# Kernel tuning notes

Measured on AMD Instinct MI355X. Metric: run time of the kernel, lower is better.

Reference implementation:

```python
import jax, jax.numpy as jnp
import numpy as np

N_NODES = 200000
N_EDGES = 400000
N_GRAPHS = 4096
H = 300
L = 5
BN_EPS = 1e-5


def setup_inputs() -> dict:
    key = jax.random.key(0)
    ks = jax.random.split(key, 12)
    s = 0.05  # weight scale for numerical stability across 5 layers
    return {
        'x': jax.random.randint(ks[0], (N_NODES, 9), 0, 120),
        'edge_index': jax.random.randint(ks[1], (2, N_EDGES), 0, N_NODES),
        'edge_attr': jax.random.randint(ks[2], (N_EDGES, 3), 0, 16),
        'batch': jnp.sort(jax.random.randint(ks[3], (N_NODES,), 0, N_GRAPHS)),
        'atom_emb': jax.random.normal(ks[4], (9, 120, H), jnp.float32) * s,
        'bond_emb': jax.random.normal(ks[5], (L, 3, 16, H), jnp.float32) * s,
        'eps': jnp.zeros((L,), jnp.float32),
        'W1': jax.random.normal(ks[6], (L, H, 2 * H), jnp.float32) * s,
        'b1': jnp.zeros((L, 2 * H), jnp.float32),
        'bn_gamma': jnp.ones((L, 2 * H), jnp.float32),
        'bn_beta': jnp.zeros((L, 2 * H), jnp.float32),
        'bn_mean': jnp.zeros((L, 2 * H), jnp.float32),
        'bn_var': jnp.ones((L, 2 * H), jnp.float32),
        'W2': jax.random.normal(ks[7], (L, 2 * H, H), jnp.float32) * s,
        'b2': jnp.zeros((L, H), jnp.float32),
        'cls_W': jax.random.normal(ks[8], (H, 2), jnp.float32) * s,
        'cls_b': jnp.zeros((2,), jnp.float32),
    }


def reference(x, edge_index, edge_attr, batch, atom_emb, bond_emb, eps,
              W1, b1, bn_gamma, bn_beta, bn_mean, bn_var, W2, b2, cls_W, cls_b):
    N = x.shape[0]
    # AtomEncoder: sum of 9 categorical embeddings -> [N, H]
    h = jnp.sum(atom_emb[jnp.arange(9)[None, :], x], axis=1)
    src, dst = edge_index[0], edge_index[1]
    feat_idx3 = jnp.arange(3)[None, :]
    for l in range(W1.shape[0]):
        # BondEncoder for this layer: sum of 3 categorical embeddings -> [E, H]
        e = jnp.sum(bond_emb[l][feat_idx3, edge_attr], axis=1)
        # message = relu(x_j + edge_emb), aggregated by scatter-add at dst
        m = jax.nn.relu(h[src] + e)
        agg = jax.ops.segment_sum(m, dst, num_segments=N)
        z = (1.0 + eps[l]) * h + agg
        # MLP: Linear(H,2H) -> BN(eval) -> ReLU -> Linear(2H,H)
        z = z @ W1[l] + b1[l]
        z = (z - bn_mean[l]) * (bn_gamma[l] * jax.lax.rsqrt(bn_var[l] + BN_EPS)) + bn_beta[l]
        z = jax.nn.relu(z)
        h = z @ W2[l] + b2[l]
    # global mean pool over graphs
    sums = jax.ops.segment_sum(h, batch, num_segments=N_GRAPHS)
    counts = jax.ops.segment_sum(jnp.ones((N, 1), h.dtype), batch, num_segments=N_GRAPHS)
    graph_feature = sums / jnp.maximum(counts, 1.0)
    logits = graph_feature @ cls_W + cls_b
    return logits, graph_feature
```

## Files before the change

### kernel.cpp

```cpp
#include <hip/hip_runtime.h>
#include <hip/hip_bf16.h>

#define N_NODES 200000
#define N_EDGES 400000
#define N_GRAPHS 4096
#define HDIM 300
#define H2DIM 600
#define NLAYERS 5

typedef __hip_bfloat16 bf16;
typedef __attribute__((ext_vector_type(4))) short s16x4;
typedef __attribute__((ext_vector_type(8))) short s16x8;
typedef __attribute__((ext_vector_type(4))) float f32x4v;

__device__ inline short f2bf(float f) {
    __hip_bfloat16 b = __float2bfloat16(f);
    return *(short*)&b;
}
__device__ inline float bf2f(short s) {
    __hip_bfloat16 b = *(__hip_bfloat16*)&s;
    return __bfloat162float(b);
}

__device__ inline void gload_lds16(const short* g, short* l) {
    __builtin_amdgcn_global_load_lds(
        (const __attribute__((address_space(1))) unsigned int*)g,
        (__attribute__((address_space(3))) unsigned int*)l,
        16, 0, 0);
}

__global__ void diag_kernel(float* __restrict__ out, int n, float val) {
    int i = blockIdx.x * blockDim.x + threadIdx.x;
    if (i < n) out[i] = val;
}

__global__ void hist_kernel(const int* __restrict__ edge_index, int* __restrict__ offs) {
    int e = blockIdx.x * blockDim.x + threadIdx.x;
    if (e >= N_EDGES) return;
    atomicAdd(&offs[edge_index[N_EDGES + e]], 1);
}

#define SCAN_N 200001
__global__ void scan1_kernel(int* __restrict__ offs, int* __restrict__ bsum) {
    __shared__ int ls[256];
    int tid = threadIdx.x;
    int base = blockIdx.x * 1024 + tid * 4;
    int v[4];
#pragma unroll
    for (int j = 0; j < 4; j++) v[j] = (base + j < SCAN_N) ? offs[base + j] : 0;
    int t = v[0] + v[1] + v[2] + v[3];
    ls[tid] = t;
    __syncthreads();
    for (int off = 1; off < 256; off <<= 1) {
        int y = (tid >= off) ? ls[tid - off] : 0;
        __syncthreads();
        ls[tid] += y;
        __syncthreads();
    }
    int ex = ls[tid] - t;
#pragma unroll
    for (int j = 0; j < 4; j++) {
        if (base + j < SCAN_N) offs[base + j] = ex;
        ex += v[j];
    }
    if (tid == 255) bsum[blockIdx.x] = ls[255];
}

__global__ void scan2_kernel(int* __restrict__ bsum, int nb) {
    __shared__ int ls[256];
    int tid = threadIdx.x;
    int v = (tid < nb) ? bsum[tid] : 0;
    ls[tid] = v;
    __syncthreads();
    for (int off = 1; off < 256; off <<= 1) {
        int y = (tid >= off) ? ls[tid - off] : 0;
        __syncthreads();
        ls[tid] += y;
        __syncthreads();
    }
    if (tid < nb) bsum[tid] = ls[tid] - v;
}

__global__ void scan3_kernel(int* __restrict__ offs, const int* __restrict__ bsum) {
    int i = blockIdx.x * blockDim.x + threadIdx.x;
    if (i >= SCAN_N) return;
    offs[i] += bsum[i >> 10];
}

__global__ void scatter_kernel(const int* __restrict__ edge_index,
                               const int* __restrict__ edge_attr,
                               int* __restrict__ offs,
                               int* __restrict__ sidx) {
    int e = blockIdx.x * blockDim.x + threadIdx.x;
    if (e >= N_EDGES) return;
    int src = edge_index[e];
    int dst = edge_index[N_EDGES + e];
    int combo = edge_attr[e * 3 + 0] | (edge_attr[e * 3 + 1] << 4) | (edge_attr[e * 3 + 2] << 8);
    int pos = atomicAdd(&offs[dst], 1);
    sidx[pos] = src | (combo << 18);
}

__global__ void etab_kernel(const float* __restrict__ bond_l, short* __restrict__ etab) {
    int idx = blockIdx.x * blockDim.x + threadIdx.x;
    if (idx >= 4096 * 304) return;
    int combo = idx / 304;
    int c = idx - combo * 304;
    if (c >= HDIM) { etab[idx] = 0; return; }
    int a0 = combo & 15, a1 = (combo >> 4) & 15, a2 = combo >> 8;
    float v = bond_l[a0 * HDIM + c] + bond_l[16 * HDIM + a1 * HDIM + c]
            + bond_l[32 * HDIM + a2 * HDIM + c];
    etab[idx] = f2bf(v);
}

__global__ void prep_w_swz(const float* __restrict__ W1, const float* __restrict__ W2,
                           short* __restrict__ Wt1s, short* __restrict__ Wt2s) {
    int idx = blockIdx.x * blockDim.x + threadIdx.x;
    const int G1 = NLAYERS * 40 * 10 * 64;
    const int G2 = NLAYERS * 20 * 20 * 64;
    if (idx < G1) {
        int l = idx / (40 * 10 * 64);
        int r = idx - l * (40 * 10 * 64);
        int nt = r / (10 * 64);
        int r2 = r - nt * (10 * 64);
        int kb = r2 >> 6;
        int lane = r2 & 63;
        int n = nt * 16 + (lane & 15);
        int k0 = kb * 32 + (lane >> 4) * 8;
        s16x8 o;
#pragma unroll
        for (int j = 0; j < 8; j++) {
            int k = k0 + j;
            float v = (n < H2DIM && k < HDIM) ? W1[((size_t)l * HDIM + k) * H2DIM + n] : 0.f;
            o[j] = f2bf(v);
        }
        *(s16x8*)&Wt1s[(size_t)idx * 8] = o;
    } else if (idx < G1 + G2) {
        int t = idx - G1;
        int l = t / (20 * 20 * 64);
        int r = t - l * (20 * 20 * 64);
        int nt = r / (20 * 64);
        int r2 = r - nt * (20 * 64);
        int kb = r2 >> 6;
        int lane = r2 & 63;
        int n = nt * 16 + (lane & 15);
        int k0 = kb * 32 + (lane >> 4) * 8;
        s16x8 o;
#pragma unroll
        for (int j = 0; j < 8; j++) {
            int k = k0 + j;
            float v = (n < HDIM && k < H2DIM) ? W2[((size_t)l * H2DIM + k) * HDIM + n] : 0.f;
            o[j] = f2bf(v);
        }
        *(s16x8*)&Wt2s[(size_t)t * 8] = o;
    }
}

__global__ void atom_kernel(const int* __restrict__ x,
                            const float* __restrict__ atom_emb,
                            short* __restrict__ h) {
    int i = blockIdx.x * blockDim.x + threadIdx.x;
    if (i >= N_NODES * 75) return;
    int n = i / 75;
    int c = (i - n * 75) * 4;
    const int* xr = x + n * 9;
    float4 s = {0.f, 0.f, 0.f, 0.f};
#pragma unroll
    for (int f = 0; f < 9; f++) {
        float4 v = *(const float4*)&atom_emb[(size_t)(f * 120 + xr[f]) * HDIM + c];
        s.x += v.x; s.y += v.y; s.z += v.z; s.w += v.w;
    }
    s16x4 o = {f2bf(s.x), f2bf(s.y), f2bf(s.z), f2bf(s.w)};
    *(s16x4*)&h[(size_t)n * HDIM + c] = o;
}

__launch_bounds__(256)
__global__ void agg_kernel(const short* __restrict__ h_in,
                           short* __restrict__ z,
                           const int* __restrict__ offs,
                           const int* __restrict__ sidx,
                           const short* __restrict__ etab,
                           const float* __restrict__ eps, int l) {
    int tid = threadIdx.x;
    int q = tid >> 4;
    int l16 = tid & 15;
    int n = blockIdx.x * 16 + q;
    float e1 = 1.f + eps[l];
    int beg = (n == 0) ? 0 : offs[n - 1];
    int end = offs[n];

    float4 acc[5];
#pragma unroll
    for (int j = 0; j < 5; j++) acc[j] = (float4){0.f, 0.f, 0.f, 0.f};
    bool tail = l16 < 11;
    int ctail = 256 + l16 * 4;

    int e = beg;
    for (; e + 2 <= end; e += 2) {
        int pk0 = sidx[e];
        int pk1 = sidx[e + 1];
        const short* hr0 = h_in + (size_t)(pk0 & 0x3FFFF) * HDIM;
        const short* er0 = etab + (((unsigned)pk0) >> 18) * 304;
        const short* hr1 = h_in + (size_t)(pk1 & 0x3FFFF) * HDIM;
        const short* er1 = etab + (((unsigned)pk1) >> 18) * 304;
        s16x4 hv0[5], ev0[5], hv1[5], ev1[5];
#pragma unroll
        for (int rep = 0; rep < 4; rep++) {
            int c = rep * 64 + l16 * 4;
            hv0[rep] = *(const s16x4*)(hr0 + c);
            ev0[rep] = *(const s16x4*)(er0 + c);
            hv1[rep] = *(const s16x4*)(hr1 + c);
            ev1[rep] = *(const s16x4*)(er1 + c);
        }
        if (tail) {
            hv0[4] = *(const s16x4*)(hr0 + ctail);
            ev0[4] = *(const s16x4*)(er0 + ctail);
            hv1[4] = *(const s16x4*)(hr1 + ctail);
            ev1[4] = *(const s16x4*)(er1 + ctail);
        }
#pragma unroll
        for (int rep = 0; rep < 5; rep++) {
            if (rep == 4 && !tail) continue;
            acc[rep].x += fmaxf(0.f, bf2f(hv0[rep].x) + bf2f(ev0[rep].x))
                        + fmaxf(0.f, bf2f(hv1[rep].x) + bf2f(ev1[rep].x));
            acc[rep].y += fmaxf(0.f, bf2f(hv0[rep].y) + bf2f(ev0[rep].y))
                        + fmaxf(0.f, bf2f(hv1[rep].y) + bf2f(ev1[rep].y));
            acc[rep].z += fmaxf(0.f, bf2f(hv0[rep].z) + bf2f(ev0[rep].z))
                        + fmaxf(0.f, bf2f(hv1[rep].z) + bf2f(ev1[rep].z));
            acc[rep].w += fmaxf(0.f, bf2f(hv0[rep].w) + bf2f(ev0[rep].w))
                        + fmaxf(0.f, bf2f(hv1[rep].w) + bf2f(ev1[rep].w));
        }
    }
    if (e < end) {
        int pk0 = sidx[e];
        const short* hr0 = h_in + (size_t)(pk0 & 0x3FFFF) * HDIM;
        const short* er0 = etab + (((unsigned)pk0) >> 18) * 304;
        s16x4 hv0[5], ev0[5];
#pragma unroll
        for (int rep = 0; rep < 4; rep++) {
            int c = rep * 64 + l16 * 4;
            hv0[rep] = *(const s16x4*)(hr0 + c);
            ev0[rep] = *(const s16x4*)(er0 + c);
        }
        if (tail) {
            hv0[4] = *(const s16x4*)(hr0 + ctail);
            ev0[4] = *(const s16x4*)(er0 + ctail);
        }
#pragma unroll
        for (int rep = 0; rep < 5; rep++) {
            if (rep == 4 && !tail) continue;
            acc[rep].x += fmaxf(0.f, bf2f(hv0[rep].x) + bf2f(ev0[rep].x));
            acc[rep].y += fmaxf(0.f, bf2f(hv0[rep].y) + bf2f(ev0[rep].y));
            acc[rep].z += fmaxf(0.f, bf2f(hv0[rep].z) + bf2f(ev0[rep].z));
            acc[rep].w += fmaxf(0.f, bf2f(hv0[rep].w) + bf2f(ev0[rep].w));
        }
    }

    const short* hn = h_in + (size_t)n * HDIM;
    short* zr = z + (size_t)n * HDIM;
#pragma unroll
    for (int rep = 0; rep < 5; rep++) {
        if (rep == 4 && !tail) continue;
        int c = rep < 4 ? rep * 64 + l16 * 4 : ctail;
        s16x4 hv = *(const s16x4*)(hn + c);
        s16x4 o;
        o.x = f2bf(fmaf(e1, bf2f(hv.x), acc[rep].x));
        o.y = f2bf(fmaf(e1, bf2f(hv.y), acc[rep].y));
        o.z = f2bf(fmaf(e1, bf2f(hv.z), acc[rep].z));
        o.w = f2bf(fmaf(e1, bf2f(hv.w), acc[rep].w));
        *(s16x4*)(zr + c) = o;
    }
}

#define ZST 328
#define WBUF_OFF (64 * ZST)
#define WBUF_SHORTS (20 * 64 * 8)
#define YS_OFF (WBUF_OFF + WBUF_SHORTS)
#define YST 136
#define LDS_SHORTS (YS_OFF + 64 * YST)

__launch_bounds__(256, 2)
__global__ void mlp_kernel(const short* __restrict__ zin,
                           short* __restrict__ hout,
                           const short* __restrict__ Wt1,
                           const short* __restrict__ Wt2,
                           const float* __restrict__ b1l,
                           const float* __restrict__ gammal,
                           const float* __restrict__ betal,
                           const float* __restrict__ meanl,
                           const float* __restrict__ varl,
                           const float* __restrict__ b2l) {
    __shared__ short lds[LDS_SHORTS];
    int tid = threadIdx.x;
    int wng = tid >> 6;
    int lane = tid & 63;
    int quad = lane >> 4;
    int l16 = lane & 15;
    int row0 = blockIdx.x * 64;

    for (int i = tid; i < 64 * 82; i += 256) {
        int r = i / 82;
        int p = (i - r * 82) * 4;
        s16x4 v = *(const s16x4*)&zin[(size_t)(row0 + r) * HDIM + p];
        *(s16x4*)&lds[r * ZST + p] = v;
    }

    f32x4v acc2[4][5];
#pragma unroll
    for (int rt = 0; rt < 4; rt++)
#pragma unroll
        for (int ct = 0; ct < 5; ct++) acc2[rt][ct] = (f32x4v){0.f, 0.f, 0.f, 0.f};

    for (int cc = 0; cc < 5; cc++) {
        f32x4v acc1[4][2];
#pragma unroll
        for (int rt = 0; rt < 4; rt++)
#pragma unroll
            for (int ct = 0; ct < 2; ct++) acc1[rt][ct] = (f32x4v){0.f, 0.f, 0.f, 0.f};

        for (int kbp = 0; kbp < 5; kbp++) {
            __syncthreads();
#pragma unroll
            for (int j = 0; j < 4; j++) {
                int c = j * 4 + wng;
                int nt_ = c >> 1, kb2 = c & 1;
                const short* src = Wt1 +
                    ((size_t)(((cc * 8 + nt_) * 10 + kbp * 2 + kb2) * 64) + lane) * 8;
                gload_lds16(src, &lds[WBUF_OFF + c * 512]);
            }
            __syncthreads();
#pragma unroll
            for (int kb2 = 0; kb2 < 2; kb2++) {
                int ks = (kbp * 2 + kb2) * 32 + quad * 8;
                s16x8 a[4];
#pragma unroll
                for (int rt = 0; rt < 4; rt++)
                    a[rt] = *(const s16x8*)&lds[(rt * 16 + l16) * ZST + ks];
#pragma unroll
                for (int ct = 0; ct < 2; ct++) {
                    int c = (wng * 2 + ct) * 2 + kb2;
                    s16x8 b = *(const s16x8*)&lds[WBUF_OFF + c * 512 + lane * 8];
#pragma unroll
                    for (int rt = 0; rt < 4; rt++)
                        acc1[rt][ct] = __builtin_amdgcn_mfma_f32_16x16x32_bf16(a[rt], b, acc1[rt][ct], 0, 0, 0);
                }
            }
        }
#pragma unroll
        for (int ct = 0; ct < 2; ct++) {
            int kc = wng * 32 + ct * 16 + l16;
            int col = cc * 128 + kc;
            bool valid = col < H2DIM;
            float s = 0.f, sh = 0.f;
            if (valid) {
                s = gammal[col] * rsqrtf(varl[col] + 1e-5f);
                sh = betal[col] + (b1l[col] - meanl[col]) * s;
            }
#pragma unroll
            for (int rt = 0; rt < 4; rt++)
#pragma unroll
                for (int rr = 0; rr < 4; rr++) {
                    float v = valid ? fmaxf(0.f, fmaf(acc1[rt][ct][rr], s, sh)) : 0.f;
                    lds[YS_OFF + (rt * 16 + quad * 4 + rr) * YST + kc] = f2bf(v);
                }
        }
#pragma unroll
        for (int kbl = 0; kbl < 4; kbl++) {
            __syncthreads();
#pragma unroll
            for (int j = 0; j < 5; j++) {
                int c = j * 4 + wng;
                const short* src = Wt2 +
                    ((size_t)((c * 20 + cc * 4 + kbl) * 64) + lane) * 8;
                gload_lds16(src, &lds[WBUF_OFF + c * 512]);
            }
            __syncthreads();
            int ks = kbl * 32 + quad * 8;
            s16x8 a[4];
#pragma unroll
            for (int rt = 0; rt < 4; rt++)
                a[rt] = *(const s16x8*)&lds[YS_OFF + (rt * 16 + l16) * YST + ks];
#pragma unroll
            for (int ct = 0; ct < 5; ct++) {
                int c = wng * 5 + ct;
                s16x8 b = *(const s16x8*)&lds[WBUF_OFF + c * 512 + lane * 8];
#pragma unroll
                for (int rt = 0; rt < 4; rt++)
                    acc2[rt][ct] = __builtin_amdgcn_mfma_f32_16x16x32_bf16(a[rt], b, acc2[rt][ct], 0, 0, 0);
            }
        }
    }
#pragma unroll
    for (int ct = 0; ct < 5; ct++) {
        int col = wng * 80 + ct * 16 + l16;
        if (col < HDIM) {
            float bb = b2l[col];
#pragma unroll
            for (int rt = 0; rt < 4; rt++)
#pragma unroll
                for (int rr = 0; rr < 4; rr++) {
                    int r = rt * 16 + quad * 4 + rr;
                    lds[r * HDIM + col] = f2bf(acc2[rt][ct][rr] + bb);
                }
        }
    }
    __syncthreads();
    for (int i = tid; i < 64 * 75; i += 256) {
        *(s16x4*)&hout[(size_t)row0 * HDIM + i * 4] = *(const s16x4*)&lds[i * 4];
    }
}

__device__ int lower_bound_dev(const int* a, int n, int v) {
    int lo = 0, hi = n;
    while (lo < hi) {
        int mid = (lo + hi) >> 1;
        if (a[mid] < v) lo = mid + 1; else hi = mid;
    }
    return lo;
}

__global__ void pool_kernel(const short* __restrict__ h,
                            const int* __restrict__ batch,
                            const float* __restrict__ cls_W,
                            const float* __restrict__ cls_b,
                            float* __restrict__ out) {
    __shared__ int seg[2];
    __shared__ float r0s[256], r1s[256];
    int g = blockIdx.x;
    int t = threadIdx.x;
    if (t == 0) {
        seg[0] = lower_bound_dev(batch, N_NODES, g);
        seg[1] = lower_bound_dev(batch, N_NODES, g + 1);
    }
    __syncthreads();
    int s = seg[0], e = seg[1];
    float inv = 1.f / fmaxf((float)(e - s), 1.f);
    float p0 = 0.f, p1 = 0.f;
    if (t < 75) {
        int c = t * 4;
        float4 sum = {0.f, 0.f, 0.f, 0.f};
        for (int n = s; n < e; n++) {
            s16x4 v = *(const s16x4*)&h[(size_t)n * HDIM + c];
            sum.x += bf2f(v.x);
            sum.y += bf2f(v.y);
            sum.z += bf2f(v.z);
            sum.w += bf2f(v.w);
        }
        float4 gf = {sum.x * inv, sum.y * inv, sum.z * inv, sum.w * inv};
        *(float4*)&out[2 * N_GRAPHS + (size_t)g * HDIM + c] = gf;
        p0 = gf.x * cls_W[c * 2] + gf.y * cls_W[(c + 1) * 2]
           + gf.z * cls_W[(c + 2) * 2] + gf.w * cls_W[(c + 3) * 2];
        p1 = gf.x * cls_W[c * 2 + 1] + gf.y * cls_W[(c + 1) * 2 + 1]
           + gf.z * cls_W[(c + 2) * 2 + 1] + gf.w * cls_W[(c + 3) * 2 + 1];
    }
    r0s[t] = p0;
    r1s[t] = p1;
    __syncthreads();
    for (int st = 128; st > 0; st >>= 1) {
        if (t < st) { r0s[t] += r0s[t + st]; r1s[t] += r1s[t + st]; }
        __syncthreads();
    }
    if (t == 0) {
        out[g * 2 + 0] = r0s[0] + cls_b[0];
        out[g * 2 + 1] = r1s[0] + cls_b[1];
    }
}

extern "C" void kernel_launch(void* const* d_in, const int* in_sizes, int n_in,
                              void* d_out, int out_size, void* d_ws, size_t ws_size,
                              hipStream_t stream) {
    const int* x          = (const int*)d_in[0];
    const int* edge_index = (const int*)d_in[1];
    const int* edge_attr  = (const int*)d_in[2];
    const int* batch      = (const int*)d_in[3];
    const float* atom_emb = (const float*)d_in[4];
    const float* bond_emb = (const float*)d_in[5];
    const float* eps      = (const float*)d_in[6];
    const float* W1       = (const float*)d_in[7];
    const float* b1       = (const float*)d_in[8];
    const float* bn_gamma = (const float*)d_in[9];
    const float* bn_beta  = (const float*)d_in[10];
    const float* bn_mean  = (const float*)d_in[11];
    const float* bn_var   = (const float*)d_in[12];
    const float* W2       = (const float*)d_in[13];
    const float* b2       = (const float*)d_in[14];
    const float* cls_W    = (const float*)d_in[15];
    const float* cls_b    = (const float*)d_in[16];
    float* out = (float*)d_out;

    char* base = (char*)d_ws;
    const size_t OFF_HA   = 0;
    const size_t OFF_HB   = 120000000;
    const size_t OFF_WT1  = 240000000;
    const size_t OFF_WT2  = 242048000;
    const size_t OFF_ETAB = 244096000;
    const size_t OFF_SIDX = 246586368;
    const size_t OFF_OFFS = 248186368;
    const size_t OFF_BSUM = 248986384;
    const size_t TOTAL    = 248987168;

    if (ws_size < TOTAL) {
        float mb = (float)(ws_size >> 20);
        diag_kernel<<<(out_size + 255) / 256, 256, 0, stream>>>(out, out_size, mb);
        return;
    }

    short* hA   = (short*)(base + OFF_HA);
    short* hB   = (short*)(base + OFF_HB);
    short* Wt1s = (short*)(base + OFF_WT1);
    short* Wt2s = (short*)(base + OFF_WT2);
    short* etab = (short*)(base + OFF_ETAB);
    int*   sidx = (int*)(base + OFF_SIDX);
    int*   offs = (int*)(base + OFF_OFFS);
    int*   bsum = (int*)(base + OFF_BSUM);

    hipMemsetAsync(offs, 0, SCAN_N * sizeof(int), stream);
    hist_kernel<<<(N_EDGES + 255) / 256, 256, 0, stream>>>(edge_index, offs);
    scan1_kernel<<<196, 256, 0, stream>>>(offs, bsum);
    scan2_kernel<<<1, 256, 0, stream>>>(bsum, 196);
    scan3_kernel<<<(SCAN_N + 255) / 256, 256, 0, stream>>>(offs, bsum);
    scatter_kernel<<<(N_EDGES + 255) / 256, 256, 0, stream>>>(edge_index, edge_attr, offs, sidx);

    {
        int total = NLAYERS * 40 * 10 * 64 + NLAYERS * 20 * 20 * 64;
        prep_w_swz<<<(total + 255) / 256, 256, 0, stream>>>(W1, W2, Wt1s, Wt2s);
    }
    atom_kernel<<<(N_NODES * 75 + 255) / 256, 256, 0, stream>>>(x, atom_emb, hA);

    for (int l = 0; l < NLAYERS; l++) {
        etab_kernel<<<(4096 * 304 + 255) / 256, 256, 0, stream>>>(
            bond_emb + (size_t)l * 3 * 16 * HDIM, etab);
        agg_kernel<<<N_NODES / 16, 256, 0, stream>>>(
            hA, hB, offs, sidx, etab, eps, l);
        mlp_kernel<<<N_NODES / 64, 256, 0, stream>>>(
            hB, hA,
            Wt1s + (size_t)l * 640 * 320, Wt2s + (size_t)l * 320 * 640,
            b1 + l * H2DIM, bn_gamma + l * H2DIM, bn_beta + l * H2DIM,
            bn_mean + l * H2DIM, bn_var + l * H2DIM, b2 + l * HDIM);
    }

    pool_kernel<<<N_GRAPHS, 256, 0, stream>>>(hA, batch, cls_W, cls_b, out);
}
```

Before: 2.406 ms.

## Double-buffer weight tiles in MLP kernel to overlap loads with MFMA

Splits the LDS weight buffer into two halves and prefetches the next weight chunk (W1 k-blocks, then W2 column halves, then the next chunk's W1) into the idle half while MFMAs run on the current half. This leaves one barrier per step instead of two and hides global-to-LDS latency across the whole GEMM1→GEMM2 chain. The W2 column tiles are remapped across waves, so wave work is uneven (some waves do 3 tiles, others 2) and there are more, smaller chunks. The extra synchronisation before the Y-tile reads also adds complexity.

After: 9.029 ms. +275.2%, slower.

```diff
diff --git a/kernel.cpp b/kernel.cpp
--- a/kernel.cpp
+++ b/kernel.cpp
@@ -273,8 +273,8 @@
 
 #define ZST 328
 #define WBUF_OFF (64 * ZST)
-#define WBUF_SHORTS (20 * 64 * 8)
-#define YS_OFF (WBUF_OFF + WBUF_SHORTS)
+#define WHALF 5120
+#define YS_OFF (WBUF_OFF + 2 * WHALF)
 #define YST 136
 #define LDS_SHORTS (YS_OFF + 64 * YST)
 
@@ -304,12 +304,21 @@
         *(s16x4*)&lds[r * ZST + p] = v;
     }
 
+#pragma unroll
+    for (int j2 = 0; j2 < 2; j2++) {
+        int c = j2 * 4 + wng;
+        const short* src = Wt1 + ((size_t)(c * 10) * 64 + lane) * 8;
+        gload_lds16(src, &lds[WBUF_OFF + c * 512]);
+    }
+    __syncthreads();
+
     f32x4v acc2[4][5];
 #pragma unroll
     for (int rt = 0; rt < 4; rt++)
 #pragma unroll
-        for (int ct = 0; ct < 5; ct++) acc2[rt][ct] = (f32x4v){0.f, 0.f, 0.f, 0.f};
-
+        for (int j = 0; j < 5; j++) acc2[rt][j] = (f32x4v){0.f, 0.f, 0.f, 0.f};
+
+    int pbuf = 0;
     for (int cc = 0; cc < 5; cc++) {
         f32x4v acc1[4][2];
 #pragma unroll
@@ -317,33 +326,42 @@
 #pragma unroll
             for (int ct = 0; ct < 2; ct++) acc1[rt][ct] = (f32x4v){0.f, 0.f, 0.f, 0.f};
 
-        for (int kbp = 0; kbp < 5; kbp++) {
-            __syncthreads();
-#pragma unroll
-            for (int j = 0; j < 4; j++) {
-                int c = j * 4 + wng;
-                int nt_ = c >> 1, kb2 = c & 1;
-                const short* src = Wt1 +
-                    ((size_t)(((cc * 8 + nt_) * 10 + kbp * 2 + kb2) * 64) + lane) * 8;
-                gload_lds16(src, &lds[WBUF_OFF + c * 512]);
+        for (int kb = 0; kb < 10; kb++) {
+            int nb = pbuf ^ 1;
+            if (kb < 9) {
+#pragma unroll
+                for (int j2 = 0; j2 < 2; j2++) {
+                    int c = j2 * 4 + wng;
+                    const short* src = Wt1 +
+                        ((size_t)(((cc * 8 + c) * 10) + kb + 1) * 64 + lane) * 8;
+                    gload_lds16(src, &lds[WBUF_OFF + nb * WHALF + c * 512]);
+                }
+            } else {
+#pragma unroll
+                for (int j2 = 0; j2 < 3; j2++) {
+                    int c = j2 * 4 + wng;
+                    if (c < 10) {
+                        const short* src = Wt2 +
+                            ((size_t)(c * 20 + cc * 4) * 64 + lane) * 8;
+                        gload_lds16(src, &lds[WBUF_OFF + nb * WHALF + c * 512]);
+                    }
+                }
+            }
+            int ks = kb * 32 + quad * 8;
+            s16x8 a[4];
+#pragma unroll
+            for (int rt = 0; rt < 4; rt++)
+                a[rt] = *(const s16x8*)&lds[(rt * 16 + l16) * ZST + ks];
+#pragma unroll
+            for (int ct = 0; ct < 2; ct++) {
+                int p = wng * 2 + ct;
+                s16x8 b = *(const s16x8*)&lds[WBUF_OFF + pbuf * WHALF + p * 512 + lane * 8];
+#pragma unroll
+                for (int rt = 0; rt < 4; rt++)
+                    acc1[rt][ct] = __builtin_amdgcn_mfma_f32_16x16x32_bf16(a[rt], b, acc1[rt][ct], 0, 0, 0);
             }
             __syncthreads();
-#pragma unroll
-            for (int kb2 = 0; kb2 < 2; kb2++) {
-                int ks = (kbp * 2 + kb2) * 32 + quad * 8;
-                s16x8 a[4];
-#pragma unroll
-                for (int rt = 0; rt < 4; rt++)
-                    a[rt] = *(const s16x8*)&lds[(rt * 16 + l16) * ZST + ks];
-#pragma unroll
-                for (int ct = 0; ct < 2; ct++) {
-                    int c = (wng * 2 + ct) * 2 + kb2;
-                    s16x8 b = *(const s16x8*)&lds[WBUF_OFF + c * 512 + lane * 8];
-#pragma unroll
-                    for (int rt = 0; rt < 4; rt++)
-                        acc1[rt][ct] = __builtin_amdgcn_mfma_f32_16x16x32_bf16(a[rt], b, acc1[rt][ct], 0, 0, 0);
-                }
-            }
+            pbuf = nb;
         }
 #pragma unroll
         for (int ct = 0; ct < 2; ct++) {
@@ -363,35 +381,57 @@
                     lds[YS_OFF + (rt * 16 + quad * 4 + rr) * YST + kc] = f2bf(v);
                 }
         }
-#pragma unroll
+        __syncthreads();
+
         for (int kbl = 0; kbl < 4; kbl++) {
-            __syncthreads();
-#pragma unroll
-            for (int j = 0; j < 5; j++) {
-                int c = j * 4 + wng;
-                const short* src = Wt2 +
-                    ((size_t)((c * 20 + cc * 4 + kbl) * 64) + lane) * 8;
-                gload_lds16(src, &lds[WBUF_OFF + c * 512]);
-            }
-            __syncthreads();
             int ks = kbl * 32 + quad * 8;
             s16x8 a[4];
 #pragma unroll
             for (int rt = 0; rt < 4; rt++)
                 a[rt] = *(const s16x8*)&lds[YS_OFF + (rt * 16 + l16) * YST + ks];
 #pragma unroll
-            for (int ct = 0; ct < 5; ct++) {
-                int c = wng * 5 + ct;
-                s16x8 b = *(const s16x8*)&lds[WBUF_OFF + c * 512 + lane * 8];
-#pragma unroll
-                for (int rt = 0; rt < 4; rt++)
-                    acc2[rt][ct] = __builtin_amdgcn_mfma_f32_16x16x32_bf16(a[rt], b, acc2[rt][ct], 0, 0, 0);
+            for (int h = 0; h < 2; h++) {
+                int nb = pbuf ^ 1;
+                bool lastChunk = (kbl == 3 && h == 1);
+                if (!lastChunk) {
+                    int nkbl = (h == 0) ? kbl : kbl + 1;
+                    int nh = (h == 0) ? 1 : 0;
+#pragma unroll
+                    for (int j2 = 0; j2 < 3; j2++) {
+                        int c = j2 * 4 + wng;
+                        if (c < 10) {
+                            const short* src = Wt2 +
+                                ((size_t)((10 * nh + c) * 20 + cc * 4 + nkbl) * 64 + lane) * 8;
+                            gload_lds16(src, &lds[WBUF_OFF + nb * WHALF + c * 512]);
+                        }
+                    }
+                } else if (cc < 4) {
+#pragma unroll
+                    for (int j2 = 0; j2 < 2; j2++) {
+                        int c = j2 * 4 + wng;
+                        const short* src = Wt1 +
+                            ((size_t)(((cc + 1) * 8 + c) * 10) * 64 + lane) * 8;
+                        gload_lds16(src, &lds[WBUF_OFF + nb * WHALF + c * 512]);
+                    }
+                }
+                int jlo, jhi;
+                if (h == 0) { jlo = 0; jhi = (wng < 2) ? 2 : 1; }
+                else        { jlo = (wng < 2) ? 3 : 2; jhi = 4; }
+                for (int j = jlo; j <= jhi; j++) {
+                    int p = 4 * j + wng - 10 * h;
+                    s16x8 b = *(const s16x8*)&lds[WBUF_OFF + pbuf * WHALF + p * 512 + lane * 8];
+#pragma unroll
+                    for (int rt = 0; rt < 4; rt++)
+                        acc2[rt][j] = __builtin_amdgcn_mfma_f32_16x16x32_bf16(a[rt], b, acc2[rt][j], 0, 0, 0);
+                }
+                __syncthreads();
+                pbuf = nb;
             }
         }
     }
 #pragma unroll
-    for (int ct = 0; ct < 5; ct++) {
-        int col = wng * 80 + ct * 16 + l16;
+    for (int j = 0; j < 5; j++) {
+        int col = (4 * j + wng) * 16 + l16;
         if (col < HDIM) {
             float bb = b2l[col];
 #pragma unroll
@@ -399,7 +439,7 @@
 #pragma unroll
                 for (int rr = 0; rr < 4; rr++) {
                     int r = rt * 16 + quad * 4 + rr;
-                    lds[r * HDIM + col] = f2bf(acc2[rt][ct][rr] + bb);
+                    lds[r * HDIM + col] = f2bf(acc2[rt][j][rr] + bb);
                 }
         }
     }
```
